# Optimization experiments

Hardware: AMD Instinct MI355X
Metric: run time of the kernel (lower is better)

Reference implementation:

```python
import jax, jax.numpy as jnp
import numpy as np

# --- static config (matches init_kwargs / input_specs) ---
N_GRAPHS = 32
NODES = 1000          # num_nodes per graph
N = N_GRAPHS * NODES  # 32000 total nodes
F_IN = 128            # num_features
E_DIM = 16            # edge_attr_dim
H, C = 4, 16          # heads, GAT_dim
HC = H * C            # 64
E = 512000            # edges (before self-loops)
PROJ = 8              # proj_nodes
OUT = 256             # output_dim
NEG_SLOPE = 0.2       # PyG GATConv default


def setup_inputs() -> dict:
    key = jax.random.key(0)
    ks = jax.random.split(key, 20)
    s = 0.1
    return {
        "x": jax.random.normal(ks[0], (N, F_IN), jnp.float32),
        "edge_attr": jax.random.normal(ks[1], (E, E_DIM), jnp.float32),
        # layer 0 (input_conv): F_IN -> H*C
        "W0":   jax.random.normal(ks[2], (F_IN, HC), jnp.float32) * s,
        "a_s0": jax.random.normal(ks[3], (H, C), jnp.float32) * s,
        "a_d0": jax.random.normal(ks[4], (H, C), jnp.float32) * s,
        "W_e0": jax.random.normal(ks[5], (E_DIM, HC), jnp.float32) * s,
        "a_e0": jax.random.normal(ks[6], (H, C), jnp.float32) * s,
        "b0":   jnp.zeros((HC,), jnp.float32),
        # layers 1..2 stacked: HC -> H*C
        "Wg":   jax.random.normal(ks[7], (2, HC, HC), jnp.float32) * s,
        "a_sg": jax.random.normal(ks[8], (2, H, C), jnp.float32) * s,
        "a_dg": jax.random.normal(ks[9], (2, H, C), jnp.float32) * s,
        "W_eg": jax.random.normal(ks[10], (2, E_DIM, HC), jnp.float32) * s,
        "a_eg": jax.random.normal(ks[11], (2, H, C), jnp.float32) * s,
        "bg":   jnp.zeros((2, HC), jnp.float32),
        # node_proj: HC -> PROJ ; fc_out: NODES*PROJ -> OUT
        "Wp": jax.random.normal(ks[12], (HC, PROJ), jnp.float32) * s,
        "bp": jnp.zeros((PROJ,), jnp.float32),
        "Wo": jax.random.normal(ks[13], (NODES * PROJ, OUT), jnp.float32) * (s / 4),
        "bo": jnp.zeros((OUT,), jnp.float32),
        "edge_index": jax.random.randint(ks[14], (2, E), 0, N, jnp.int32),
        "batch": jnp.repeat(jnp.arange(N_GRAPHS, dtype=jnp.int32), NODES),
    }


def _gat_layer(x, src, dst, eattr, W, a_s, a_d, W_e, a_e, b):
    """PyG GATConv (concat=True, shared src/dst lin, edge_dim) forward."""
    xl = (x @ W).reshape(N, H, C)                       # [N,H,C]
    al_s = jnp.sum(xl * a_s, axis=-1)                   # [N,H]
    al_d = jnp.sum(xl * a_d, axis=-1)                   # [N,H]
    el = (eattr @ W_e).reshape(-1, H, C)                # [Ef,H,C]
    al_e = jnp.sum(el * a_e, axis=-1)                   # [Ef,H]
    logits = jax.nn.leaky_relu(al_s[src] + al_d[dst] + al_e, NEG_SLOPE)
    # segment softmax over destination nodes (every node has a self-loop)
    mx = jax.ops.segment_max(logits, dst, num_segments=N)
    p = jnp.exp(logits - mx[dst])
    denom = jax.ops.segment_sum(p, dst, num_segments=N)
    alpha = p / denom[dst]                               # [Ef,H]
    out = jax.ops.segment_sum(xl[src] * alpha[..., None], dst, num_segments=N)
    return out.reshape(N, HC) + b


def reference(x, edge_attr, W0, a_s0, a_d0, W_e0, a_e0, b0,
              Wg, a_sg, a_dg, W_eg, a_eg, bg,
              Wp, bp, Wo, bo, edge_index, batch):
    src, dst = edge_index[0], edge_index[1]
    # PyG add_self_loops with fill_value='mean': per-dst mean of incoming edge_attr
    deg = jax.ops.segment_sum(jnp.ones((E,), edge_attr.dtype), dst, num_segments=N)
    loop_attr = jax.ops.segment_sum(edge_attr, dst, num_segments=N) / jnp.maximum(deg, 1.0)[:, None]
    loops = jnp.arange(N, dtype=src.dtype)
    src_f = jnp.concatenate([src, loops])
    dst_f = jnp.concatenate([dst, loops])
    ea_f = jnp.concatenate([edge_attr, loop_attr], axis=0)   # [E+N, E_DIM]

    h = jax.nn.relu(_gat_layer(x, src_f, dst_f, ea_f, W0, a_s0, a_d0, W_e0, a_e0, b0))
    for i in range(2):
        h = jax.nn.relu(_gat_layer(h, src_f, dst_f, ea_f,
                                   Wg[i], a_sg[i], a_dg[i], W_eg[i], a_eg[i], bg[i]))
    h = jax.nn.relu(h @ Wp + bp)                             # [N, PROJ]
    B = batch.shape[0] // NODES                              # static batch count
    h = h.reshape(B, NODES * PROJ)
    return h @ Wo + bo                                       # [B, OUT]
```

## Files before the change

kernel.cpp:

```cpp
#include <hip/hip_runtime.h>
#include <hip/hip_bf16.h>
#include <hip/hip_fp16.h>

#define N_NODES 32000
#define FIN     128
#define E_EDGES 512000
#define EF_EDGES 544000
#define HC      64
#define XSTR    72
#define NGRAPH  32
#define PROJ    8
#define OUT_DIM 256

static __device__ inline unsigned short f2bf(float f) {
  unsigned int x = __float_as_uint(f);
  unsigned int r = (x + 0x7fffu + ((x >> 16) & 1u)) >> 16;
  return (unsigned short)r;
}
static __device__ inline float bf2f(unsigned short u) {
  return __uint_as_float((unsigned int)u << 16);
}
static __device__ inline unsigned short f2h(float f) {
  return __half_as_ushort(__float2half(f));
}
static __device__ inline float h2f(unsigned short u) {
  return __half2float(__ushort_as_half(u));
}

__global__ __launch_bounds__(256) void zero_kernel(int* __restrict__ deg) {
  deg[blockIdx.x * 256 + threadIdx.x] = 0;
}

__global__ __launch_bounds__(256) void deg_kernel(const int* __restrict__ ei,
                                                  int* __restrict__ deg) {
  int e = blockIdx.x * 256 + threadIdx.x;
  atomicAdd(&deg[ei[E_EDGES + e]], 1);
}

__global__ __launch_bounds__(256) void scan1_kernel(const int* __restrict__ deg,
                                                    int* __restrict__ offs,
                                                    int* __restrict__ bsum) {
  int idx = blockIdx.x * 256 + threadIdx.x;
  int lane = threadIdx.x & 63;
  int w = threadIdx.x >> 6;
  int v = deg[idx] + 1;
  int s = v;
#pragma unroll
  for (int off = 1; off < 64; off <<= 1) {
    int t = __shfl_up(s, off);
    if (lane >= off) s += t;
  }
  __shared__ int wsum[4];
  if (lane == 63) wsum[w] = s;
  __syncthreads();
  int add = 0;
#pragma unroll
  for (int i = 0; i < 4; ++i) add += (i < w) ? wsum[i] : 0;
  int incl = s + add;
  offs[idx] = incl - v;
  if (threadIdx.x == 255) bsum[blockIdx.x] = incl;
}

__global__ __launch_bounds__(256) void scan3_kernel(const int* __restrict__ bsum,
                                                    int* __restrict__ offs,
                                                    int* __restrict__ nxt) {
  __shared__ int wsum[4];
  int tid = threadIdx.x, bid = blockIdx.x;
  int lane = tid & 63, w = tid >> 6;
  int v = (tid < bid) ? bsum[tid] : 0;
#pragma unroll
  for (int off = 1; off < 64; off <<= 1) v += __shfl_xor(v, off);
  if (lane == 0) wsum[w] = v;
  __syncthreads();
  int boff = wsum[0] + wsum[1] + wsum[2] + wsum[3];
  int idx = bid * 256 + tid;
  int o = offs[idx] + boff;
  offs[idx] = o;
  nxt[idx] = o;
  if (bid == 0 && tid == 0) offs[N_NODES] = EF_EDGES;
}

__global__ __launch_bounds__(256) void fill_kernel(const int* __restrict__ ei,
                                                   int* __restrict__ nxt,
                                                   int* __restrict__ csr_src,
                                                   int* __restrict__ csr_eid) {
  int e = blockIdx.x * 256 + threadIdx.x;
  int s, d;
  if (e < E_EDGES) { s = ei[e]; d = ei[E_EDGES + e]; }
  else             { s = e - E_EDGES; d = s; }
  int pos = atomicAdd(&nxt[d], 1);
  csr_src[pos] = s;
  csr_eid[pos] = e;
}

__device__ __forceinline__ void compute_Me(float (*sMe)[16][4],
                                           const float* __restrict__ W_e0,
                                           const float* __restrict__ a_e0,
                                           const float* __restrict__ W_eg,
                                           const float* __restrict__ a_eg) {
  int tid = threadIdx.x;
  if (tid < 192) {
    int l = tid >> 6, r6 = tid & 63, d = r6 >> 2, h = r6 & 3;
    const float* We = (l == 0) ? W_e0 : W_eg + (size_t)(l - 1) * 16 * HC;
    const float* ae = (l == 0) ? a_e0 : a_eg + (size_t)(l - 1) * 64;
    float s = 0.f;
#pragma unroll
    for (int c = 0; c < 16; ++c) s += We[d * HC + h * 16 + c] * ae[h * 16 + c];
    sMe[l][d][h] = s;
  }
  __syncthreads();
}

__global__ __launch_bounds__(256) void edge_kernel(const float* __restrict__ edge_attr,
                                                   const float* __restrict__ W_e0,
                                                   const float* __restrict__ a_e0,
                                                   const float* __restrict__ W_eg,
                                                   const float* __restrict__ a_eg,
                                                   const int* __restrict__ offs,
                                                   const int* __restrict__ csr_eid,
                                                   unsigned short* __restrict__ lgE) {
  __shared__ float sMe[3][16][4];
  __shared__ float sMean[4][16];
  compute_Me(sMe, W_e0, a_e0, W_eg, a_eg);
  int b = blockIdx.x;
  int tid = threadIdx.x;
  if (b < 8000) {
    int lane = tid & 63, wv = tid >> 6;
    int n = b * 4 + wv;
    int k = lane & 15, g = lane >> 4;
    int beg = offs[n], end = offs[n + 1];
    float s = 0.f;
    int posl = -1;
    for (int i = beg + g; i < end; i += 4) {
      int e = csr_eid[i];
      if (e < E_EDGES) s += edge_attr[(size_t)e * 16 + k];
      else posl = i;
    }
    s += __shfl_xor(s, 16);
    s += __shfl_xor(s, 32);
    posl = max(posl, __shfl_xor(posl, 16));
    posl = max(posl, __shfl_xor(posl, 32));
    int degv = end - beg - 1;
    float mean = s / fmaxf((float)degv, 1.f);
    if (g == 0) sMean[wv][k] = mean;
    if (lane < 3) {
      int l = lane;
      float r0 = 0.f, r1 = 0.f, r2 = 0.f, r3 = 0.f;
#pragma unroll
      for (int d = 0; d < 16; ++d) {
        float a = sMean[wv][d];
        r0 = fmaf(a, sMe[l][d][0], r0);
        r1 = fmaf(a, sMe[l][d][1], r1);
        r2 = fmaf(a, sMe[l][d][2], r2);
        r3 = fmaf(a, sMe[l][d][3], r3);
      }
      unsigned long long u =
          (unsigned long long)f2h(r0) |
          ((unsigned long long)f2h(r1) << 16) |
          ((unsigned long long)f2h(r2) << 32) |
          ((unsigned long long)f2h(r3) << 48);
      *(unsigned long long*)&lgE[((size_t)l * EF_EDGES + posl) * 4] = u;
    }
  } else {
    int pos = (b - 8000) * 256 + tid;
    int e = csr_eid[pos];
    if (e < E_EDGES) {
      float av[16];
      *(float4*)&av[0]  = *(const float4*)&edge_attr[(size_t)e * 16 + 0];
      *(float4*)&av[4]  = *(const float4*)&edge_attr[(size_t)e * 16 + 4];
      *(float4*)&av[8]  = *(const float4*)&edge_attr[(size_t)e * 16 + 8];
      *(float4*)&av[12] = *(const float4*)&edge_attr[(size_t)e * 16 + 12];
#pragma unroll
      for (int l = 0; l < 3; ++l) {
        float r0 = 0.f, r1 = 0.f, r2 = 0.f, r3 = 0.f;
#pragma unroll
        for (int d = 0; d < 16; ++d) {
          float a = av[d];
          r0 = fmaf(a, sMe[l][d][0], r0);
          r1 = fmaf(a, sMe[l][d][1], r1);
          r2 = fmaf(a, sMe[l][d][2], r2);
          r3 = fmaf(a, sMe[l][d][3], r3);
        }
        unsigned long long u =
            (unsigned long long)f2h(r0) |
            ((unsigned long long)f2h(r1) << 16) |
            ((unsigned long long)f2h(r2) << 32) |
            ((unsigned long long)f2h(r3) << 48);
        __builtin_nontemporal_store(
            u, (unsigned long long*)&lgE[((size_t)l * EF_EDGES + pos) * 4]);
      }
    }
  }
}

template <int K>
__global__ __launch_bounds__(256) void transform_kernel(const float* __restrict__ A,
                                                        const float* __restrict__ W,
                                                        const float* __restrict__ a_s,
                                                        const float* __restrict__ a_d,
                                                        unsigned short* __restrict__ xlb,
                                                        float* __restrict__ al_d) {
  __shared__ float sW[64][64];
  __shared__ float sA[64][65];
  int tid = threadIdx.x;
  int row0 = blockIdx.x * 64;
  int tx = tid & 15, ty = tid >> 4;
  int c0 = tx * 4, r0 = ty * 4;
  float acc[4][4] = {};
  for (int kc = 0; kc < K; kc += 64) {
    for (int i = tid; i < 1024; i += 256) {
      int kk = i >> 4, c4 = (i & 15) * 4;
      *(float4*)&sW[kk][c4] = *(const float4*)&W[(size_t)(kc + kk) * HC + c4];
    }
    for (int i = tid; i < 1024; i += 256) {
      int r = i >> 4, k4 = (i & 15) * 4;
      float4 v = *(const float4*)&A[(size_t)(row0 + r) * K + kc + k4];
      sA[r][k4 + 0] = v.x; sA[r][k4 + 1] = v.y;
      sA[r][k4 + 2] = v.z; sA[r][k4 + 3] = v.w;
    }
    __syncthreads();
#pragma unroll 8
    for (int kk = 0; kk < 64; ++kk) {
      float4 w = *(float4*)&sW[kk][c0];
      float a0 = sA[r0 + 0][kk];
      float a1 = sA[r0 + 1][kk];
      float a2 = sA[r0 + 2][kk];
      float a3 = sA[r0 + 3][kk];
      acc[0][0] = fmaf(a0, w.x, acc[0][0]); acc[0][1] = fmaf(a0, w.y, acc[0][1]);
      acc[0][2] = fmaf(a0, w.z, acc[0][2]); acc[0][3] = fmaf(a0, w.w, acc[0][3]);
      acc[1][0] = fmaf(a1, w.x, acc[1][0]); acc[1][1] = fmaf(a1, w.y, acc[1][1]);
      acc[1][2] = fmaf(a1, w.z, acc[1][2]); acc[1][3] = fmaf(a1, w.w, acc[1][3]);
      acc[2][0] = fmaf(a2, w.x, acc[2][0]); acc[2][1] = fmaf(a2, w.y, acc[2][1]);
      acc[2][2] = fmaf(a2, w.z, acc[2][2]); acc[2][3] = fmaf(a2, w.w, acc[2][3]);
      acc[3][0] = fmaf(a3, w.x, acc[3][0]); acc[3][1] = fmaf(a3, w.y, acc[3][1]);
      acc[3][2] = fmaf(a3, w.z, acc[3][2]); acc[3][3] = fmaf(a3, w.w, acc[3][3]);
    }
    __syncthreads();
  }
  float asv[4], adv[4];
#pragma unroll
  for (int j = 0; j < 4; ++j) { asv[j] = a_s[c0 + j]; adv[j] = a_d[c0 + j]; }
  int hd = tx >> 2;
#pragma unroll
  for (int i = 0; i < 4; ++i) {
    int r = row0 + r0 + i;
    ushort4 u = make_ushort4(f2bf(acc[i][0]), f2bf(acc[i][1]),
                             f2bf(acc[i][2]), f2bf(acc[i][3]));
    *(ushort4*)&xlb[(size_t)r * XSTR + c0] = u;
    float ps = acc[i][0] * asv[0] + acc[i][1] * asv[1] + acc[i][2] * asv[2] + acc[i][3] * asv[3];
    float pd = acc[i][0] * adv[0] + acc[i][1] * adv[1] + acc[i][2] * adv[2] + acc[i][3] * adv[3];
    ps += __shfl_xor(ps, 1); ps += __shfl_xor(ps, 2);
    pd += __shfl_xor(pd, 1); pd += __shfl_xor(pd, 2);
    if ((tx & 3) == 0) {
      *(float*)&xlb[(size_t)r * XSTR + 64 + hd * 2] = ps;
      al_d[(size_t)r * 4 + hd] = pd;
    }
  }
}

template <int FUSE_PROJ>
__global__ __launch_bounds__(256, 4) void gather_kernel(const int* __restrict__ offs,
                                                        const int* __restrict__ csr_src,
                                                        const unsigned short* __restrict__ lg,
                                                        const unsigned short* __restrict__ xlb,
                                                        const float* __restrict__ al_d,
                                                        const float* __restrict__ bias,
                                                        const float* __restrict__ Wp,
                                                        const float* __restrict__ bp,
                                                        float* __restrict__ outp) {
  int tid = threadIdx.x;
  int lane = tid & 63;
  int n = blockIdx.x * 4 + (tid >> 6);
  int u = lane & 31;
  int hf = lane >> 5;
  int c0 = u * 2;
  int hd = u >> 3;
  int beg = offs[n], end = offs[n + 1];
  float ald = al_d[(size_t)n * 4 + hd];
  float denom = 0.f, a0 = 0.f, a1 = 0.f;
  for (int ib = beg; ib < end; ib += 16) {
    int sq[8]; unsigned short gq[8]; float pm[8];
#pragma unroll
    for (int q = 0; q < 8; ++q) {
      int j = ib + hf + q * 2;
      bool ok = j < end;
      int jc = ok ? j : beg;
      sq[q] = csr_src[jc];
      gq[q] = lg[(size_t)jc * 4 + hd];
      pm[q] = ok ? 1.f : 0.f;
    }
    __builtin_amdgcn_sched_barrier(0);
    unsigned int xq[8]; float alsq[8];
#pragma unroll
    for (int q = 0; q < 8; ++q) {
      const unsigned short* row = &xlb[(size_t)sq[q] * XSTR];
      xq[q] = *(const unsigned int*)&row[c0];
      alsq[q] = *(const float*)&row[64 + hd * 2];
    }
    __builtin_amdgcn_sched_barrier(0);
#pragma unroll
    for (int q = 0; q < 8; ++q) {
      float l = h2f(gq[q]) + alsq[q] + ald;
      l = (l > 0.f) ? l : 0.2f * l;
      float p = pm[q] * __expf(l);
      denom += p;
      a0 = fmaf(p, bf2f((unsigned short)(xq[q] & 0xffff)), a0);
      a1 = fmaf(p, bf2f((unsigned short)(xq[q] >> 16)), a1);
    }
  }
  denom += __shfl_xor(denom, 32);
  a0 += __shfl_xor(a0, 32);
  a1 += __shfl_xor(a1, 32);
  float hv0 = fmaxf(a0 / denom + bias[c0], 0.f);
  float hv1 = fmaxf(a1 / denom + bias[c0 + 1], 0.f);
  if constexpr (!FUSE_PROJ) {
    if (hf == 0) {
      float2 o; o.x = hv0; o.y = hv1;
      *(float2*)&outp[(size_t)n * HC + c0] = o;
    }
  } else {
    float pj[8];
#pragma unroll
    for (int j = 0; j < 8; ++j)
      pj[j] = (hf == 0) ? hv0 * Wp[c0 * PROJ + j] + hv1 * Wp[(c0 + 1) * PROJ + j] : 0.f;
#pragma unroll
    for (int off = 1; off < 64; off <<= 1) {
#pragma unroll
      for (int j = 0; j < 8; ++j) pj[j] += __shfl_xor(pj[j], off);
    }
    if (lane < 8) {
      float v = pj[0];
      v = (lane == 1) ? pj[1] : v;
      v = (lane == 2) ? pj[2] : v;
      v = (lane == 3) ? pj[3] : v;
      v = (lane == 4) ? pj[4] : v;
      v = (lane == 5) ? pj[5] : v;
      v = (lane == 6) ? pj[6] : v;
      v = (lane == 7) ? pj[7] : v;
      outp[(size_t)n * PROJ + lane] = fmaxf(v + bp[lane], 0.f);
    }
  }
}

__global__ __launch_bounds__(256) void fc1_kernel(const float* __restrict__ p,
                                                  const float* __restrict__ Wo,
                                                  float* __restrict__ part) {
  __shared__ float sp[NGRAPH][250];
  int kc = blockIdx.x;
  int ct = blockIdx.y;
  int tid = threadIdx.x;
  for (int i = tid; i < NGRAPH * 250; i += 256) {
    int g = i / 250, kk = i % 250;
    sp[g][kk] = p[(size_t)g * 8000 + kc * 250 + kk];
  }
  __syncthreads();
  int c = ct * 64 + (tid & 63);
  int kg = tid >> 6;
  float acc[NGRAPH] = {};
  for (int kk = kg; kk < 250; kk += 4) {
    float w = __builtin_nontemporal_load(&Wo[(size_t)(kc * 250 + kk) * OUT_DIM + c]);
#pragma unroll
    for (int g = 0; g < NGRAPH; ++g) acc[g] = fmaf(sp[g][kk], w, acc[g]);
  }
  int ch = kc * 4 + kg;
#pragma unroll
  for (int g = 0; g < NGRAPH; ++g)
    part[((size_t)ch * NGRAPH + g) * OUT_DIM + c] = acc[g];
}

__global__ __launch_bounds__(256) void fc2_kernel(const float* __restrict__ part,
                                                  const float* __restrict__ bo,
                                                  float* __restrict__ out) {
  int i = blockIdx.x * 256 + threadIdx.x;
  int g = i >> 8, c = i & 255;
  float s = bo[c];
  for (int ch = 0; ch < 128; ++ch) s += part[((size_t)ch * NGRAPH + g) * OUT_DIM + c];
  out[i] = s;
}

extern "C" void kernel_launch(void* const* d_in, const int* in_sizes, int n_in,
                              void* d_out, int out_size, void* d_ws, size_t ws_size,
                              hipStream_t stream) {
  const float* x         = (const float*)d_in[0];
  const float* edge_attr = (const float*)d_in[1];
  const float* W0        = (const float*)d_in[2];
  const float* a_s0      = (const float*)d_in[3];
  const float* a_d0      = (const float*)d_in[4];
  const float* W_e0      = (const float*)d_in[5];
  const float* a_e0      = (const float*)d_in[6];
  const float* b0        = (const float*)d_in[7];
  const float* Wg        = (const float*)d_in[8];
  const float* a_sg      = (const float*)d_in[9];
  const float* a_dg      = (const float*)d_in[10];
  const float* W_eg      = (const float*)d_in[11];
  const float* a_eg      = (const float*)d_in[12];
  const float* bg        = (const float*)d_in[13];
  const float* Wp        = (const float*)d_in[14];
  const float* bp        = (const float*)d_in[15];
  const float* Wo        = (const float*)d_in[16];
  const float* bo        = (const float*)d_in[17];
  const int*   ei        = (const int*)d_in[18];

  char* base = (char*)d_ws;
  size_t off = 0;
  auto alloc = [&](size_t bytes) -> void* {
    void* ptr = base + off;
    off = (off + bytes + 255) & ~(size_t)255;
    return ptr;
  };
  int*            deg     = (int*)alloc((size_t)N_NODES * 4);
  int*            offs    = (int*)alloc((size_t)(N_NODES + 1) * 4);
  int*            nxt     = (int*)alloc((size_t)N_NODES * 4);
  int*            bsum    = (int*)alloc(128 * 4);
  int*            csr_src = (int*)alloc((size_t)EF_EDGES * 4);
  int*            csr_eid = (int*)alloc((size_t)EF_EDGES * 4);
  unsigned short* lgE     = (unsigned short*)alloc((size_t)3 * EF_EDGES * 4 * 2);
  unsigned short* xlb     = (unsigned short*)alloc((size_t)N_NODES * XSTR * 2);
  float*          al_d    = (float*)alloc((size_t)N_NODES * 4 * 4);
  float*          hA      = (float*)alloc((size_t)N_NODES * HC * 4);
  float*          hB      = (float*)alloc((size_t)N_NODES * HC * 4);
  float*          pbuf    = (float*)alloc((size_t)N_NODES * PROJ * 4);
  float*          part    = (float*)alloc((size_t)128 * NGRAPH * OUT_DIM * 4);

  zero_kernel<<<N_NODES / 256, 256, 0, stream>>>(deg);
  deg_kernel<<<E_EDGES / 256, 256, 0, stream>>>(ei, deg);
  scan1_kernel<<<N_NODES / 256, 256, 0, stream>>>(deg, offs, bsum);
  scan3_kernel<<<N_NODES / 256, 256, 0, stream>>>(bsum, offs, nxt);
  fill_kernel<<<EF_EDGES / 256, 256, 0, stream>>>(ei, nxt, csr_src, csr_eid);
  edge_kernel<<<8000 + 2125, 256, 0, stream>>>(edge_attr, W_e0, a_e0, W_eg, a_eg,
                                               offs, csr_eid, lgE);
  transform_kernel<FIN><<<N_NODES / 64, 256, 0, stream>>>(x, W0, a_s0, a_d0, xlb, al_d);

  gather_kernel<0><<<N_NODES / 4, 256, 0, stream>>>(offs, csr_src, lgE, xlb,
                                                    al_d, b0, Wp, bp, hA);
  transform_kernel<HC><<<N_NODES / 64, 256, 0, stream>>>(hA, Wg, a_sg, a_dg, xlb, al_d);
  gather_kernel<0><<<N_NODES / 4, 256, 0, stream>>>(offs, csr_src, lgE + (size_t)EF_EDGES * 4,
                                                    xlb, al_d, bg, Wp, bp, hB);
  transform_kernel<HC><<<N_NODES / 64, 256, 0, stream>>>(hB, Wg + HC * HC, a_sg + 64,
                                                         a_dg + 64, xlb, al_d);
  gather_kernel<1><<<N_NODES / 4, 256, 0, stream>>>(offs, csr_src, lgE + (size_t)2 * EF_EDGES * 4,
                                                    xlb, al_d, bg + 64, Wp, bp, pbuf);

  fc1_kernel<<<dim3(32, 4), 256, 0, stream>>>(pbuf, Wo, part);
  fc2_kernel<<<NGRAPH, 256, 0, stream>>>(part, bo, (float*)d_out);
}
```

Measured before the change: 277.2 us.

## Stage gathered neighbor rows into LDS via direct global-to-LDS loads

```diff
diff --git a/kernel.cpp b/kernel.cpp
--- a/kernel.cpp
+++ b/kernel.cpp
@@ -259,58 +259,69 @@
 }
 
 template <int FUSE_PROJ>
-__global__ __launch_bounds__(256, 4) void gather_kernel(const int* __restrict__ offs,
-                                                        const int* __restrict__ csr_src,
-                                                        const unsigned short* __restrict__ lg,
-                                                        const unsigned short* __restrict__ xlb,
-                                                        const float* __restrict__ al_d,
-                                                        const float* __restrict__ bias,
-                                                        const float* __restrict__ Wp,
-                                                        const float* __restrict__ bp,
-                                                        float* __restrict__ outp) {
+__global__ __launch_bounds__(256) void gather_kernel(const int* __restrict__ offs,
+                                                     const int* __restrict__ csr_src,
+                                                     const unsigned short* __restrict__ lg,
+                                                     const unsigned short* __restrict__ xlb,
+                                                     const float* __restrict__ al_d,
+                                                     const float* __restrict__ bias,
+                                                     const float* __restrict__ Wp,
+                                                     const float* __restrict__ bp,
+                                                     float* __restrict__ outp) {
+  __shared__ char ldsraw[4 * 3072];
   int tid = threadIdx.x;
-  int lane = tid & 63;
-  int n = blockIdx.x * 4 + (tid >> 6);
+  int lane = tid & 63, wv = tid >> 6;
+  int n = blockIdx.x * 4 + wv;
   int u = lane & 31;
   int hf = lane >> 5;
-  int c0 = u * 2;
   int hd = u >> 3;
+  char* wbuf = ldsraw + wv * 3072;
   int beg = offs[n], end = offs[n + 1];
   float ald = al_d[(size_t)n * 4 + hd];
   float denom = 0.f, a0 = 0.f, a1 = 0.f;
-  for (int ib = beg; ib < end; ib += 16) {
-    int sq[8]; unsigned short gq[8]; float pm[8];
+  for (int jb = beg; jb < end; jb += 16) {
+#pragma unroll
+    for (int k = 0; k < 3; ++k) {
+      int d16 = k * 64 + lane;
+      d16 = (d16 < 144) ? d16 : 0;
+      int e = (d16 * 57) >> 9;
+      int o = d16 - e * 9;
+      int j = jb + e;
+      j = (j < end) ? j : beg;
+      int s = csr_src[j];
+      const unsigned short* g = &xlb[(size_t)s * XSTR + o * 8];
+      __builtin_amdgcn_global_load_lds(
+          (const __attribute__((address_space(1))) void*)g,
+          (__attribute__((address_space(3))) void*)(wbuf + k * 1024), 16, 0, 0);
+    }
+    unsigned short gq[8]; float pm[8];
 #pragma unroll
     for (int q = 0; q < 8; ++q) {
-      int j = ib + hf + q * 2;
+      int j = jb + q * 2 + hf;
       bool ok = j < end;
       int jc = ok ? j : beg;
-      sq[q] = csr_src[jc];
       gq[q] = lg[(size_t)jc * 4 + hd];
       pm[q] = ok ? 1.f : 0.f;
     }
+    asm volatile("s_waitcnt vmcnt(0)" ::: "memory");
     __builtin_amdgcn_sched_barrier(0);
-    unsigned int xq[8]; float alsq[8];
 #pragma unroll
     for (int q = 0; q < 8; ++q) {
-      const unsigned short* row = &xlb[(size_t)sq[q] * XSTR];
-      xq[q] = *(const unsigned int*)&row[c0];
-      alsq[q] = *(const float*)&row[64 + hd * 2];
-    }
-    __builtin_amdgcn_sched_barrier(0);
-#pragma unroll
-    for (int q = 0; q < 8; ++q) {
-      float l = h2f(gq[q]) + alsq[q] + ald;
+      int e = q * 2 + hf;
+      unsigned int xx = *(const unsigned int*)(wbuf + e * 144 + u * 4);
+      float als = *(const float*)(wbuf + e * 144 + 128 + hd * 4);
+      float l = h2f(gq[q]) + als + ald;
       l = (l > 0.f) ? l : 0.2f * l;
       float p = pm[q] * __expf(l);
       denom += p;
-      a0 = fmaf(p, bf2f((unsigned short)(xq[q] & 0xffff)), a0);
-      a1 = fmaf(p, bf2f((unsigned short)(xq[q] >> 16)), a1);
+      a0 = fmaf(p, bf2f((unsigned short)(xx & 0xffff)), a0);
+      a1 = fmaf(p, bf2f((unsigned short)(xx >> 16)), a1);
     }
   }
   denom += __shfl_xor(denom, 32);
   a0 += __shfl_xor(a0, 32);
   a1 += __shfl_xor(a1, 32);
+  int c0 = u * 2;
   float hv0 = fmaxf(a0 / denom + bias[c0], 0.f);
   float hv1 = fmaxf(a1 / denom + bias[c0 + 1], 0.f);
   if constexpr (!FUSE_PROJ) {
```

Result: no change. 279.4 us (+0.8%).
